# Kernel optimization log

Measured on AMD Instinct MI355X. Metric: run time of the kernel, lower is better.

Reference implementation:

```python
import jax, jax.numpy as jnp
import numpy as np

KH, KW = 7, 7
H, W = 4096, 4096

def setup_inputs() -> dict:
    key = jax.random.key(0)
    k1, k2 = jax.random.split(key)
    x = jax.random.normal(k1, (H, W), dtype=jnp.float32)
    weight = jax.random.normal(k2, (KH, KW), dtype=jnp.float32) * 0.001
    bias = jnp.zeros((1,), dtype=jnp.float32)
    return {"x": x, "weight": weight, "bias": bias}

def reference(x, weight, bias):
    # Single-channel valid 2D cross-correlation + scalar bias.
    # lax.conv_general_dilated performs cross-correlation (no kernel flip),
    # matching the torch loop: res[i,j] = sum(x[i:i+kh, j:j+kw] * k).
    lhs = x[None, None, :, :]            # [N=1, C=1, H, W]
    rhs = weight[None, None, :, :]       # [O=1, I=1, kh, kw]
    out = jax.lax.conv_general_dilated(
        lhs, rhs,
        window_strides=(1, 1),
        padding="VALID",
        dimension_numbers=("NCHW", "OIHW", "NCHW"),
    )
    return out[0, 0] + bias[0]           # [H-kh+1, W-kw+1]
```

## Files before the change

kernel.cpp:

```cpp
#include <hip/hip_runtime.h>
#include <stdint.h>

#define IH 4096
#define IW 4096
#define OH 4090
#define OW 4090

#define TW 256
#define TH 16
#define LW 272
#define LH 22
#define NV4 68
#define NLD (LH * NV4)
#define STEPS 4

typedef float v2f __attribute__((ext_vector_type(2)));
typedef __attribute__((address_space(1))) void gas_void;
typedef __attribute__((address_space(3))) void las_void;

__device__ __forceinline__ void stage_tile(const float* __restrict__ x,
                                           int tile_y0, int tile_x0,
                                           float* sbuf, int tid)
{
    const int wv = tid >> 6;
#pragma unroll
    for (int i = 0; i < (NLD + 255) / 256; ++i) {
        const int f = tid + i * 256;
        if (f < NLD) {
            const int r  = f / NV4;
            const int c4 = f - r * NV4;
            int iy = tile_y0 + r;
            iy = iy < IH ? iy : IH - 1;
            int c0 = tile_x0 + 4 * c4;
            c0 = c0 <= IW - 4 ? c0 : IW - 4;
            const float* gp = x + (size_t)iy * IW + c0;
            float* lp = sbuf + (size_t)(i * 256 + wv * 64) * 4;
            __builtin_amdgcn_global_load_lds((gas_void*)gp, (las_void*)lp, 16, 0, 0);
        }
    }
}

__global__ __launch_bounds__(256) void conv7x7_kernel(
    const float* __restrict__ x,
    const float* __restrict__ w,
    const float* __restrict__ bias,
    float* __restrict__ out)
{
    __shared__ float smem[2][LH * LW];

    const int tid     = threadIdx.x;
    const int tile_x0 = blockIdx.x * TW;
    const int ytile0  = blockIdx.y * STEPS;

    float wt[49];
#pragma unroll
    for (int k = 0; k < 49; ++k) wt[k] = w[k];
    const float b = bias[0];

    stage_tile(x, ytile0 * TH, tile_x0, smem[0], tid);

    const int tx  = tid & 63;
    const int wv  = tid >> 6;
    const int lx0 = 4 * tx;

    for (int s = 0; s < STEPS; ++s) {
        __syncthreads();
        if (s + 1 < STEPS)
            stage_tile(x, (ytile0 + s + 1) * TH, tile_x0, smem[(s + 1) & 1], tid);

        const float* sb = smem[s & 1];

        float acc[4][4];
#pragma unroll
        for (int r = 0; r < 4; ++r)
#pragma unroll
            for (int c = 0; c < 4; ++c) acc[r][c] = b;

#pragma unroll
        for (int ir = 0; ir < 10; ++ir) {
            const float* srow = sb + (4 * wv + ir) * LW + lx0;
            const float4 q0 = *(const float4*)(srow);
            const float4 q1 = *(const float4*)(srow + 4);
            const float4 q2 = *(const float4*)(srow + 8);
            float rb[12];
            rb[0]=q0.x; rb[1]=q0.y; rb[2]=q0.z;  rb[3]=q0.w;
            rb[4]=q1.x; rb[5]=q1.y; rb[6]=q1.z;  rb[7]=q1.w;
            rb[8]=q2.x; rb[9]=q2.y; rb[10]=q2.z; rb[11]=q2.w;

#pragma unroll
            for (int ky = 0; ky < 7; ++ky) {
                const int ry = ir - ky;
                if (ry >= 0 && ry < 4) {
#pragma unroll
                    for (int kx = 0; kx < 7; ++kx) {
                        const float wv_ = wt[ky * 7 + kx];
#pragma unroll
                        for (int c = 0; c < 4; ++c)
                            acc[ry][c] += wv_ * rb[kx + c];
                    }
                }
            }
        }

        const int ox0 = tile_x0 + lx0;
        const int oyb = (ytile0 + s) * TH + 4 * wv;
#pragma unroll
        for (int ry = 0; ry < 4; ++ry) {
            const int oy = oyb + ry;
            if (oy < OH) {
                float* orow = out + (size_t)oy * OW;
                if (ox0 + 3 < OW) {
                    v2f v0 = { acc[ry][0], acc[ry][1] };
                    v2f v1 = { acc[ry][2], acc[ry][3] };
                    __builtin_nontemporal_store(v0, (v2f*)(orow + ox0));
                    __builtin_nontemporal_store(v1, (v2f*)(orow + ox0 + 2));
                } else {
#pragma unroll
                    for (int c = 0; c < 4; ++c)
                        if (ox0 + c < OW) orow[ox0 + c] = acc[ry][c];
                }
            }
        }
    }
}

extern "C" void kernel_launch(void* const* d_in, const int* in_sizes, int n_in,
                              void* d_out, int out_size, void* d_ws, size_t ws_size,
                              hipStream_t stream) {
    const float* x    = (const float*)d_in[0];
    const float* w    = (const float*)d_in[1];
    const float* bias = (const float*)d_in[2];
    float* out        = (float*)d_out;

    dim3 grid((OW + TW - 1) / TW, (4096 / TH) / STEPS);
    conv7x7_kernel<<<grid, dim3(256), 0, stream>>>(x, w, bias, out);
}
```

Before: 128.7 us.

## Replace LDS-staged tiling with direct global loads and 8-row register blocking

Drops the double-buffered shared-memory staging through global_load_lds. Each thread now reads its input rows straight from global memory into a three-row register ring, prefetching two rows ahead. Each thread computes 8 output rows instead of 4, so every loaded row is reused across more rows. The grid shrinks to one 32-row band per block with launch bounds targeting 4 blocks per CU. This removes LDS traffic and barriers, but relies on L1/L2 to absorb overlapping horizontal loads, raises register pressure, and drops the multi-step per-block loop.

After: 249.2 us. +93.6%, slower.

```diff
diff --git a/kernel.cpp b/kernel.cpp
--- a/kernel.cpp
+++ b/kernel.cpp
@@ -6,119 +6,88 @@
 #define OH 4090
 #define OW 4090
 
-#define TW 256
-#define TH 16
-#define LW 272
-#define LH 22
-#define NV4 68
-#define NLD (LH * NV4)
-#define STEPS 4
+typedef float v2f __attribute__((ext_vector_type(2)));
 
-typedef float v2f __attribute__((ext_vector_type(2)));
-typedef __attribute__((address_space(1))) void gas_void;
-typedef __attribute__((address_space(3))) void las_void;
-
-__device__ __forceinline__ void stage_tile(const float* __restrict__ x,
-                                           int tile_y0, int tile_x0,
-                                           float* sbuf, int tid)
-{
-    const int wv = tid >> 6;
-#pragma unroll
-    for (int i = 0; i < (NLD + 255) / 256; ++i) {
-        const int f = tid + i * 256;
-        if (f < NLD) {
-            const int r  = f / NV4;
-            const int c4 = f - r * NV4;
-            int iy = tile_y0 + r;
-            iy = iy < IH ? iy : IH - 1;
-            int c0 = tile_x0 + 4 * c4;
-            c0 = c0 <= IW - 4 ? c0 : IW - 4;
-            const float* gp = x + (size_t)iy * IW + c0;
-            float* lp = sbuf + (size_t)(i * 256 + wv * 64) * 4;
-            __builtin_amdgcn_global_load_lds((gas_void*)gp, (las_void*)lp, 16, 0, 0);
-        }
-    }
-}
-
-__global__ __launch_bounds__(256) void conv7x7_kernel(
+__global__ __launch_bounds__(256, 4) void conv7x7_direct(
     const float* __restrict__ x,
     const float* __restrict__ w,
     const float* __restrict__ bias,
     float* __restrict__ out)
 {
-    __shared__ float smem[2][LH * LW];
+    const int tid  = threadIdx.x;
+    const int tx   = tid & 63;
+    const int band = tid >> 6;
 
-    const int tid     = threadIdx.x;
-    const int tile_x0 = blockIdx.x * TW;
-    const int ytile0  = blockIdx.y * STEPS;
+    const int x0  = blockIdx.x * 256 + 4 * tx;
+    const int oy0 = blockIdx.y * 32 + band * 8;
 
     float wt[49];
 #pragma unroll
     for (int k = 0; k < 49; ++k) wt[k] = w[k];
     const float b = bias[0];
 
-    stage_tile(x, ytile0 * TH, tile_x0, smem[0], tid);
+    const int c1 = (x0 + 4 <= IW - 4) ? x0 + 4 : IW - 4;
+    const int c2 = (x0 + 8 <= IW - 4) ? x0 + 8 : IW - 4;
 
-    const int tx  = tid & 63;
-    const int wv  = tid >> 6;
-    const int lx0 = 4 * tx;
+    float acc[8][4];
+#pragma unroll
+    for (int r = 0; r < 8; ++r)
+#pragma unroll
+        for (int c = 0; c < 4; ++c) acc[r][c] = b;
 
-    for (int s = 0; s < STEPS; ++s) {
-        __syncthreads();
-        if (s + 1 < STEPS)
-            stage_tile(x, (ytile0 + s + 1) * TH, tile_x0, smem[(s + 1) & 1], tid);
+    float buf[3][12];
 
-        const float* sb = smem[s & 1];
+#define LOADROW(dst, IR) do {                                              \
+        int iy_ = oy0 + (IR);                                              \
+        iy_ = iy_ < IH ? iy_ : IH - 1;                   \
+        const float* rp_ = x + ((size_t)iy_ << 12);                        \
+        const float4 a_ = *(const float4*)(rp_ + x0);                      \
+        const float4 b_ = *(const float4*)(rp_ + c1);                      \
+        const float4 q_ = *(const float4*)(rp_ + c2);                      \
+        dst[0] = a_.x; dst[1] = a_.y; dst[2]  = a_.z; dst[3]  = a_.w;      \
+        dst[4] = b_.x; dst[5] = b_.y; dst[6]  = b_.z; dst[7]  = b_.w;      \
+        dst[8] = q_.x; dst[9] = q_.y; dst[10] = q_.z; dst[11] = q_.w;      \
+    } while (0)
 
-        float acc[4][4];
-#pragma unroll
-        for (int r = 0; r < 4; ++r)
-#pragma unroll
-            for (int c = 0; c < 4; ++c) acc[r][c] = b;
+    LOADROW(buf[0], 0);
+    LOADROW(buf[1], 1);
 
 #pragma unroll
-        for (int ir = 0; ir < 10; ++ir) {
-            const float* srow = sb + (4 * wv + ir) * LW + lx0;
-            const float4 q0 = *(const float4*)(srow);
-            const float4 q1 = *(const float4*)(srow + 4);
-            const float4 q2 = *(const float4*)(srow + 8);
-            float rb[12];
-            rb[0]=q0.x; rb[1]=q0.y; rb[2]=q0.z;  rb[3]=q0.w;
-            rb[4]=q1.x; rb[5]=q1.y; rb[6]=q1.z;  rb[7]=q1.w;
-            rb[8]=q2.x; rb[9]=q2.y; rb[10]=q2.z; rb[11]=q2.w;
+    for (int ir = 0; ir < 14; ++ir) {
+        if (ir + 2 < 14) LOADROW(buf[(ir + 2) % 3], ir + 2);
+
+        const float* rb = buf[ir % 3];
 
 #pragma unroll
-            for (int ky = 0; ky < 7; ++ky) {
-                const int ry = ir - ky;
-                if (ry >= 0 && ry < 4) {
+        for (int ky = 0; ky < 7; ++ky) {
+            const int ry = ir - ky;
+            if (ry >= 0 && ry < 8) {
 #pragma unroll
-                    for (int kx = 0; kx < 7; ++kx) {
-                        const float wv_ = wt[ky * 7 + kx];
+                for (int kx = 0; kx < 7; ++kx) {
+                    const float ww = wt[ky * 7 + kx];
 #pragma unroll
-                        for (int c = 0; c < 4; ++c)
-                            acc[ry][c] += wv_ * rb[kx + c];
-                    }
+                    for (int c = 0; c < 4; ++c)
+                        acc[ry][c] += ww * rb[kx + c];
                 }
             }
         }
+    }
+#undef LOADROW
 
-        const int ox0 = tile_x0 + lx0;
-        const int oyb = (ytile0 + s) * TH + 4 * wv;
 #pragma unroll
-        for (int ry = 0; ry < 4; ++ry) {
-            const int oy = oyb + ry;
-            if (oy < OH) {
-                float* orow = out + (size_t)oy * OW;
-                if (ox0 + 3 < OW) {
-                    v2f v0 = { acc[ry][0], acc[ry][1] };
-                    v2f v1 = { acc[ry][2], acc[ry][3] };
-                    __builtin_nontemporal_store(v0, (v2f*)(orow + ox0));
-                    __builtin_nontemporal_store(v1, (v2f*)(orow + ox0 + 2));
-                } else {
+    for (int ry = 0; ry < 8; ++ry) {
+        const int oy = oy0 + ry;
+        if (oy < OH) {
+            float* orow = out + (size_t)oy * OW + x0;
+            if (x0 + 3 < OW) {
+                v2f v0 = { acc[ry][0], acc[ry][1] };
+                v2f v1 = { acc[ry][2], acc[ry][3] };
+                __builtin_nontemporal_store(v0, (v2f*)orow);
+                __builtin_nontemporal_store(v1, (v2f*)(orow + 2));
+            } else {
 #pragma unroll
-                    for (int c = 0; c < 4; ++c)
-                        if (ox0 + c < OW) orow[ox0 + c] = acc[ry][c];
-                }
+                for (int c = 0; c < 4; ++c)
+                    if (x0 + c < OW) orow[c] = acc[ry][c];
             }
         }
     }
@@ -132,6 +101,6 @@
     const float* bias = (const float*)d_in[2];
     float* out        = (float*)d_out;
 
-    dim3 grid((OW + TW - 1) / TW, (4096 / TH) / STEPS);
-    conv7x7_kernel<<<grid, dim3(256), 0, stream>>>(x, w, bias, out);
+    dim3 grid((OW + 255) / 256, (OH + 31) / 32);
+    conv7x7_direct<<<grid, dim3(256), 0, stream>>>(x, w, bias, out);
 }
```

## Replace double-buffered tiles with a rolling LDS row ring for halo reuse

Applied to the files above, without the earlier changes.

Switches from double-buffered 22-row tiles, which reload the 6-row halo each step, to a 22-slot ring buffer of input rows. Each step loads only the 8 new rows, so the halo is reused across steps. Per-thread output drops from 4x4 to 2x4, which lowers registers and allows more waves per CU (launch bounds of 4). The trade-off is more shared-memory reads per output, since each thread now reads 8 rows to produce 2. It also adds a hand-placed vmcnt wait and barrier whose correctness depends on how many loads are still in flight.

Result: slower. 227.2 us (+76.5%).

```diff
diff --git a/kernel.cpp b/kernel.cpp
--- a/kernel.cpp
+++ b/kernel.cpp
@@ -7,78 +7,87 @@
 #define OW 4090
 
 #define TW 256
-#define TH 16
+#define TH 8
+#define STEPS 8
+#define RING 22
 #define LW 272
-#define LH 22
-#define NV4 68
-#define NLD (LH * NV4)
-#define STEPS 4
+#define YB (TH * STEPS)
 
 typedef float v2f __attribute__((ext_vector_type(2)));
 typedef __attribute__((address_space(1))) void gas_void;
 typedef __attribute__((address_space(3))) void las_void;
 
-__device__ __forceinline__ void stage_tile(const float* __restrict__ x,
-                                           int tile_y0, int tile_x0,
-                                           float* sbuf, int tid)
+
+__device__ __forceinline__ void stage_row(const float* __restrict__ x,
+                                          int iy, int slot, int tile_x0,
+                                          float* smem, int tx)
 {
-    const int wv = tid >> 6;
-#pragma unroll
-    for (int i = 0; i < (NLD + 255) / 256; ++i) {
-        const int f = tid + i * 256;
-        if (f < NLD) {
-            const int r  = f / NV4;
-            const int c4 = f - r * NV4;
-            int iy = tile_y0 + r;
-            iy = iy < IH ? iy : IH - 1;
-            int c0 = tile_x0 + 4 * c4;
-            c0 = c0 <= IW - 4 ? c0 : IW - 4;
-            const float* gp = x + (size_t)iy * IW + c0;
-            float* lp = sbuf + (size_t)(i * 256 + wv * 64) * 4;
-            __builtin_amdgcn_global_load_lds((gas_void*)gp, (las_void*)lp, 16, 0, 0);
-        }
-    }
+    iy = iy < IH ? iy : IH - 1;
+    const float* gr = x + ((size_t)iy << 12);
+    int c0 = tile_x0 + 4 * tx;
+    c0 = c0 <= IW - 4 ? c0 : IW - 4;
+    float* lp = smem + slot * LW;
+    __builtin_amdgcn_global_load_lds((gas_void*)(gr + c0), (las_void*)lp, 16, 0, 0);
+    int c1 = tile_x0 + 256 + 4 * tx;
+    c1 = c1 <= IW - 4 ? c1 : IW - 4;
+    if (tx < 4)
+        __builtin_amdgcn_global_load_lds((gas_void*)(gr + c1), (las_void*)(lp + 256), 16, 0, 0);
 }
 
-__global__ __launch_bounds__(256) void conv7x7_kernel(
+__global__ __launch_bounds__(256, 4) void conv7x7_ring(
     const float* __restrict__ x,
     const float* __restrict__ w,
     const float* __restrict__ bias,
     float* __restrict__ out)
 {
-    __shared__ float smem[2][LH * LW];
+    __shared__ float smem[RING * LW];
 
-    const int tid     = threadIdx.x;
+    const int tid = threadIdx.x;
+    const int tx  = tid & 63;
+    const int wv  = tid >> 6;
     const int tile_x0 = blockIdx.x * TW;
-    const int ytile0  = blockIdx.y * STEPS;
+    const int y0 = blockIdx.y * YB;
 
     float wt[49];
 #pragma unroll
     for (int k = 0; k < 49; ++k) wt[k] = w[k];
     const float b = bias[0];
 
-    stage_tile(x, ytile0 * TH, tile_x0, smem[0], tid);
+#pragma unroll
+    for (int rr = 0; rr < 4; ++rr) {
+        const int r = wv + 4 * rr;
+        if (r < 14)
+            stage_row(x, y0 + r, r, tile_x0, smem, tx);
+    }
+    __syncthreads();
 
-    const int tx  = tid & 63;
-    const int wv  = tid >> 6;
     const int lx0 = 4 * tx;
+    int base_slot = 0;
 
+#pragma unroll 1
     for (int s = 0; s < STEPS; ++s) {
-        __syncthreads();
-        if (s + 1 < STEPS)
-            stage_tile(x, (ytile0 + s + 1) * TH, tile_x0, smem[(s + 1) & 1], tid);
+        if (s + 1 < STEPS) {
+#pragma unroll
+            for (int j2 = 0; j2 < 2; ++j2) {
+                const int j = 2 * wv + j2;
+                int sl = base_slot + 14 + j;
+                if (sl >= RING) sl -= RING;
+                stage_row(x, y0 + TH * s + 14 + j, sl, tile_x0, smem, tx);
+            }
+        }
 
-        const float* sb = smem[s & 1];
-
-        float acc[4][4];
+        float acc[2][4];
 #pragma unroll
-        for (int r = 0; r < 4; ++r)
+        for (int r = 0; r < 2; ++r)
 #pragma unroll
             for (int c = 0; c < 4; ++c) acc[r][c] = b;
 
+        const int slot0 = base_slot + 2 * wv;
 #pragma unroll
-        for (int ir = 0; ir < 10; ++ir) {
-            const float* srow = sb + (4 * wv + ir) * LW + lx0;
+        for (int ir = 0; ir < 8; ++ir) {
+            int sl = slot0 + ir;
+            if (sl >= RING) sl -= RING;
+            const float* srow = smem + sl * LW + lx0;
             const float4 q0 = *(const float4*)(srow);
             const float4 q1 = *(const float4*)(srow + 4);
             const float4 q2 = *(const float4*)(srow + 8);
@@ -90,37 +99,46 @@
 #pragma unroll
             for (int ky = 0; ky < 7; ++ky) {
                 const int ry = ir - ky;
-                if (ry >= 0 && ry < 4) {
+                if (ry >= 0 && ry < 2) {
 #pragma unroll
                     for (int kx = 0; kx < 7; ++kx) {
-                        const float wv_ = wt[ky * 7 + kx];
+                        const float ww = wt[ky * 7 + kx];
 #pragma unroll
                         for (int c = 0; c < 4; ++c)
-                            acc[ry][c] += wv_ * rb[kx + c];
+                            acc[ry][c] += ww * rb[kx + c];
                     }
                 }
             }
         }
 
         const int ox0 = tile_x0 + lx0;
-        const int oyb = (ytile0 + s) * TH + 4 * wv;
 #pragma unroll
-        for (int ry = 0; ry < 4; ++ry) {
-            const int oy = oyb + ry;
+        for (int ry = 0; ry < 2; ++ry) {
+            const int oy = y0 + TH * s + 2 * wv + ry;
             if (oy < OH) {
-                float* orow = out + (size_t)oy * OW;
+                float* orow = out + (size_t)oy * OW + ox0;
                 if (ox0 + 3 < OW) {
                     v2f v0 = { acc[ry][0], acc[ry][1] };
                     v2f v1 = { acc[ry][2], acc[ry][3] };
-                    __builtin_nontemporal_store(v0, (v2f*)(orow + ox0));
-                    __builtin_nontemporal_store(v1, (v2f*)(orow + ox0 + 2));
+                    __builtin_nontemporal_store(v0, (v2f*)orow);
+                    __builtin_nontemporal_store(v1, (v2f*)(orow + 2));
                 } else {
 #pragma unroll
                     for (int c = 0; c < 4; ++c)
-                        if (ox0 + c < OW) orow[ox0 + c] = acc[ry][c];
+                        if (ox0 + c < OW) orow[c] = acc[ry][c];
                 }
             }
         }
+
+        if (s + 1 < STEPS) {
+            asm volatile("s_waitcnt vmcnt(2)" ::: "memory");
+            __builtin_amdgcn_sched_barrier(0);
+            __builtin_amdgcn_s_barrier();
+            __builtin_amdgcn_sched_barrier(0);
+            asm volatile("" ::: "memory");
+        }
+        base_slot += TH;
+        if (base_slot >= RING) base_slot -= RING;
     }
 }
 
@@ -132,6 +150,6 @@
     const float* bias = (const float*)d_in[2];
     float* out        = (float*)d_out;
 
-    dim3 grid((OW + TW - 1) / TW, (4096 / TH) / STEPS);
-    conv7x7_kernel<<<grid, dim3(256), 0, stream>>>(x, w, bias, out);
+    dim3 grid((OW + TW - 1) / TW, (OH + YB - 1) / YB);
+    conv7x7_ring<<<grid, dim3(256), 0, stream>>>(x, w, bias, out);
 }
```
